# Optimization experiments

Hardware: AMD Instinct MI355X
Metric: run time of the kernel (lower is better)

Reference implementation:

```python
import jax, jax.numpy as jnp
import numpy as np

B, C, T, D = 4, 248, 500, 64


def setup_inputs() -> dict:
    key = jax.random.key(0)
    ks = jax.random.split(key, 7)
    scale = 1.0  # nn.Linear(1, d) default init is U(-1, 1); exact dist irrelevant for correctness baseline
    return {
        "x": jax.random.normal(ks[0], (B, C, T), dtype=jnp.float32),
        "wq": jax.random.uniform(ks[1], (D,), jnp.float32, -scale, scale),
        "bq": jax.random.uniform(ks[2], (D,), jnp.float32, -scale, scale),
        "wk": jax.random.uniform(ks[3], (D,), jnp.float32, -scale, scale),
        "bk": jax.random.uniform(ks[4], (D,), jnp.float32, -scale, scale),
        "wv": jax.random.uniform(ks[5], (D,), jnp.float32, -scale, scale),
        "bv": jax.random.uniform(ks[6], (D,), jnp.float32, -scale, scale),
    }


def reference(x, wq, bq, wk, bk, wv, bv):
    # x: [B, C, T] -> xt: [B, T, C]; each scalar projected to attn_dim D
    xt = jnp.transpose(x, (0, 2, 1))
    Q = xt[..., None] * wq + bq            # [B, T, C, D]
    K = xt[..., None] * wk + bk            # [B, T, C, D]
    V = xt[..., None] * wv + bv            # [B, T, C, D]
    d = Q.shape[-1]
    # channel-wise attention per (B, T) slice
    scores = jnp.einsum("btcd,bted->btce", Q, K) / jnp.sqrt(jnp.float32(d))
    wts = jax.nn.softmax(scores, axis=-1)  # [B, T, C, C] (dropout=0 / eval mode)
    out = jnp.einsum("btce,bted->btcd", wts, V).mean(axis=2)  # [B, T, D]
    return out, wts
```

## Files before the change

### kernel.cpp

```cpp
#include <hip/hip_runtime.h>
#include <math.h>

#define BB 4
#define CC 248
#define TT 500
#define DD 64

__device__ __forceinline__ float waveReduceSum(float v) {
    #pragma unroll
    for (int off = 32; off > 0; off >>= 1) v += __shfl_xor(v, off, 64);
    return v;
}

__global__ __launch_bounds__(256) void csa_kernel(
    const float* __restrict__ x,
    const float* __restrict__ wq, const float* __restrict__ bq,
    const float* __restrict__ wk, const float* __restrict__ bk,
    const float* __restrict__ wv, const float* __restrict__ bv,
    float* __restrict__ out, float* __restrict__ wts)
{
    const int bt = blockIdx.x;
    const int b  = bt / TT;
    const int t  = bt % TT;
    const int tid  = threadIdx.x;
    const int wave = tid >> 6;
    const int lane = tid & 63;

    __shared__ __align__(16) float xs[CC];
    __shared__ float sred[8];
    __shared__ float sA, sB2, sXmax, sXmin, sYbar;

    if (tid < CC) xs[tid] = x[((size_t)b * CC + tid) * TT + t];

    if (wave == 1) {
        float wkv = wk[lane];
        float pa = wq[lane] * wkv;
        float pb = bq[lane] * wkv;
        #pragma unroll
        for (int off = 32; off > 0; off >>= 1) {
            pa += __shfl_xor(pa, off, 64);
            pb += __shfl_xor(pb, off, 64);
        }
        if (lane == 0) { sA = pa * 0.125f; sB2 = pb * 0.125f; }
    }
    __syncthreads();

    float vmax = -INFINITY, vmin = INFINITY;
    if (tid < CC) { vmax = xs[tid]; vmin = xs[tid]; }
    #pragma unroll
    for (int off = 32; off > 0; off >>= 1) {
        vmax = fmaxf(vmax, __shfl_xor(vmax, off, 64));
        vmin = fminf(vmin, __shfl_xor(vmin, off, 64));
    }
    if (lane == 0) { sred[wave] = vmax; sred[4 + wave] = vmin; }
    __syncthreads();
    if (tid == 0) {
        sXmax = fmaxf(fmaxf(sred[0], sred[1]), fmaxf(sred[2], sred[3]));
        sXmin = fminf(fminf(sred[4], sred[5]), fminf(sred[6], sred[7]));
    }
    __syncthreads();

    const float a    = sA;
    const float b2   = sB2;
    const float xmax = sXmax;
    const float xmin = sXmin;
    const float4* xs4 = reinterpret_cast<const float4*>(xs);

    float4 xv = make_float4(0.f, 0.f, 0.f, 0.f);
    const bool active = (lane < CC / 4);
    if (active) xv = xs4[lane];

    float ywave = 0.f;
    const size_t slice = (size_t)bt * CC * CC;

    for (int c = wave; c < CC; c += 4) {
        const float sc = fmaf(a, xs[c], b2);
        const float m  = (sc >= 0.f) ? sc * xmax : sc * xmin;

        float4 p = make_float4(0.f, 0.f, 0.f, 0.f);
        float sum = 0.f, xp = 0.f;
        if (active) {
            p.x = __expf(fmaf(sc, xv.x, -m));
            p.y = __expf(fmaf(sc, xv.y, -m));
            p.z = __expf(fmaf(sc, xv.z, -m));
            p.w = __expf(fmaf(sc, xv.w, -m));
            sum = (p.x + p.y) + (p.z + p.w);
            xp  = (p.x * xv.x + p.y * xv.y) + (p.z * xv.z + p.w * xv.w);
        }
        const float denom = waveReduceSum(sum);
        const float xps   = waveReduceSum(xp);
        const float inv   = 1.0f / denom;

        if (active) {
            float4 o;
            o.x = p.x * inv; o.y = p.y * inv; o.z = p.z * inv; o.w = p.w * inv;
            reinterpret_cast<float4*>(wts + slice + (size_t)c * CC)[lane] = o;
        }
        ywave += xps * inv;
    }

    if (lane == 0) sred[wave] = ywave;
    __syncthreads();
    if (tid == 0)
        sYbar = (sred[0] + sred[1] + sred[2] + sred[3]) * (1.0f / CC);
    __syncthreads();

    if (tid < DD)
        out[(size_t)bt * DD + tid] = fmaf(wv[tid], sYbar, bv[tid]);
}

extern "C" void kernel_launch(void* const* d_in, const int* in_sizes, int n_in,
                              void* d_out, int out_size, void* d_ws, size_t ws_size,
                              hipStream_t stream) {
    const float* x  = (const float*)d_in[0];
    const float* wq = (const float*)d_in[1];
    const float* bq = (const float*)d_in[2];
    const float* wk = (const float*)d_in[3];
    const float* bk = (const float*)d_in[4];
    const float* wv = (const float*)d_in[5];
    const float* bv = (const float*)d_in[6];

    float* out = (float*)d_out;
    float* wts = (float*)d_out + (size_t)BB * TT * DD;

    csa_kernel<<<dim3(BB * TT), dim3(256), 0, stream>>>(x, wq, bq, wk, bk, wv, bv, out, wts);
}
```

Measured before the change: 118.5 us.

## Process two softmax rows per wave with half-wave reductions and exp2

Each wave now splits into two 32-lane halves that each handle one row of the channel-attention softmax, with every lane holding 8 columns instead of 4. This removes the idle lanes from the old 62-of-64 lane mapping and cuts the cross-lane shuffle reductions per row from six steps to five. The score scale is premultiplied by log2(e) so that exp2 can be used directly, and the reciprocal of the sum uses the hardware rcp instead of a full division, which trades a little accuracy for fewer instructions. The loop is unrolled by 2, which may raise register use.

```diff
diff --git a/kernel.cpp b/kernel.cpp
--- a/kernel.cpp
+++ b/kernel.cpp
@@ -6,11 +6,7 @@
 #define TT 500
 #define DD 64
 
-__device__ __forceinline__ float waveReduceSum(float v) {
-    #pragma unroll
-    for (int off = 32; off > 0; off >>= 1) v += __shfl_xor(v, off, 64);
-    return v;
-}
+typedef float f32x4 __attribute__((ext_vector_type(4)));
 
 __global__ __launch_bounds__(256) void csa_kernel(
     const float* __restrict__ x,
@@ -25,6 +21,8 @@
     const int tid  = threadIdx.x;
     const int wave = tid >> 6;
     const int lane = tid & 63;
+    const int q    = lane & 31;
+    const int h    = lane >> 5;
 
     __shared__ __align__(16) float xs[CC];
     __shared__ float sred[8];
@@ -46,7 +44,7 @@
     __syncthreads();
 
     float vmax = -INFINITY, vmin = INFINITY;
-    if (tid < CC) { vmax = xs[tid]; vmin = xs[tid]; }
+    if (tid < CC) { vmax = xs[tid]; vmin = vmax; }
     #pragma unroll
     for (int off = 32; off > 0; off >>= 1) {
         vmax = fmaxf(vmax, __shfl_xor(vmax, off, 64));
@@ -60,49 +58,67 @@
     }
     __syncthreads();
 
-    const float a    = sA;
-    const float b2   = sB2;
+    const float LOG2E = 1.4426950408889634f;
+    const float a2   = sA  * LOG2E;
+    const float b22  = sB2 * LOG2E;
     const float xmax = sXmax;
     const float xmin = sXmin;
-    const float4* xs4 = reinterpret_cast<const float4*>(xs);
 
-    float4 xv = make_float4(0.f, 0.f, 0.f, 0.f);
-    const bool active = (lane < CC / 4);
-    if (active) xv = xs4[lane];
+    const f32x4* xs4 = reinterpret_cast<const f32x4*>(xs);
+    const bool act = (q < 31);
+    f32x4 xlo = {0.f,0.f,0.f,0.f}, xhi = {0.f,0.f,0.f,0.f};
+    if (act) { xlo = xs4[q]; xhi = xs4[31 + q]; }
 
-    float ywave = 0.f;
-    const size_t slice = (size_t)bt * CC * CC;
+    float ysum = 0.f;
+    const size_t slice = (size_t)bt * (CC * CC);
 
-    for (int c = wave; c < CC; c += 4) {
-        const float sc = fmaf(a, xs[c], b2);
-        const float m  = (sc >= 0.f) ? sc * xmax : sc * xmin;
+    #pragma unroll 2
+    for (int i = 0; i < 31; ++i) {
+        const int r = 8 * i + 2 * wave + h;
+        const float scl = fmaf(a2, xs[r], b22);
+        const float ml  = (scl >= 0.f) ? scl * xmax : scl * xmin;
 
-        float4 p = make_float4(0.f, 0.f, 0.f, 0.f);
+        f32x4 plo = {0.f,0.f,0.f,0.f}, phi = {0.f,0.f,0.f,0.f};
         float sum = 0.f, xp = 0.f;
-        if (active) {
-            p.x = __expf(fmaf(sc, xv.x, -m));
-            p.y = __expf(fmaf(sc, xv.y, -m));
-            p.z = __expf(fmaf(sc, xv.z, -m));
-            p.w = __expf(fmaf(sc, xv.w, -m));
-            sum = (p.x + p.y) + (p.z + p.w);
-            xp  = (p.x * xv.x + p.y * xv.y) + (p.z * xv.z + p.w * xv.w);
+        if (act) {
+            plo.x = __builtin_amdgcn_exp2f(fmaf(scl, xlo.x, -ml));
+            plo.y = __builtin_amdgcn_exp2f(fmaf(scl, xlo.y, -ml));
+            plo.z = __builtin_amdgcn_exp2f(fmaf(scl, xlo.z, -ml));
+            plo.w = __builtin_amdgcn_exp2f(fmaf(scl, xlo.w, -ml));
+            phi.x = __builtin_amdgcn_exp2f(fmaf(scl, xhi.x, -ml));
+            phi.y = __builtin_amdgcn_exp2f(fmaf(scl, xhi.y, -ml));
+            phi.z = __builtin_amdgcn_exp2f(fmaf(scl, xhi.z, -ml));
+            phi.w = __builtin_amdgcn_exp2f(fmaf(scl, xhi.w, -ml));
+            sum = ((plo.x + plo.y) + (plo.z + plo.w)) + ((phi.x + phi.y) + (phi.z + phi.w));
+            xp  = ((plo.x * xlo.x + plo.y * xlo.y) + (plo.z * xlo.z + plo.w * xlo.w))
+                + ((phi.x * xhi.x + phi.y * xhi.y) + (phi.z * xhi.z + phi.w * xhi.w));
         }
-        const float denom = waveReduceSum(sum);
-        const float xps   = waveReduceSum(xp);
-        const float inv   = 1.0f / denom;
+        #pragma unroll
+        for (int off = 16; off > 0; off >>= 1) {
+            sum += __shfl_xor(sum, off, 64);
+            xp  += __shfl_xor(xp,  off, 64);
+        }
+        const float inv = __builtin_amdgcn_rcpf(sum);
 
-        if (active) {
-            float4 o;
-            o.x = p.x * inv; o.y = p.y * inv; o.z = p.z * inv; o.w = p.w * inv;
-            reinterpret_cast<float4*>(wts + slice + (size_t)c * CC)[lane] = o;
+        if (act) {
+            f32x4 olo, ohi;
+            olo.x = plo.x * inv; olo.y = plo.y * inv; olo.z = plo.z * inv; olo.w = plo.w * inv;
+            ohi.x = phi.x * inv; ohi.y = phi.y * inv; ohi.z = phi.z * inv; ohi.w = phi.w * inv;
+            f32x4* dst = reinterpret_cast<f32x4*>(wts + slice + (size_t)r * CC);
+            dst[q]      = olo;
+            dst[31 + q] = ohi;
         }
-        ywave += xps * inv;
+        ysum += xp * inv;
     }
 
-    if (lane == 0) sred[wave] = ywave;
+    if (q == 0) sred[wave * 2 + h] = ysum;
     __syncthreads();
-    if (tid == 0)
-        sYbar = (sred[0] + sred[1] + sred[2] + sred[3]) * (1.0f / CC);
+    if (tid == 0) {
+        float s = 0.f;
+        #pragma unroll
+        for (int k = 0; k < 8; ++k) s += sred[k];
+        sYbar = s * (1.0f / CC);
+    }
     __syncthreads();
 
     if (tid < DD)
```

Measured after the change: 104.5 us. 1.13x faster.

## Compute softmax row stats per thread, then write weights in a flat coalesced pass

Applied to the files above, without the earlier changes.

Each thread now owns one softmax row and computes its max-shifted denominator and weighted x sum serially over channels, with no per-row wave reductions. The row parameters go to shared memory, and a second flat pass recomputes the exponentials and writes the weight matrix contiguously using all lanes. It also switches to exp2 with a pre-scaled log2e and a hardware reciprocal. The cost is computing exponentials twice and reading from LDS with divide-by-62 indexing.

```diff
diff --git a/kernel.cpp b/kernel.cpp
--- a/kernel.cpp
+++ b/kernel.cpp
@@ -5,12 +5,9 @@
 #define CC 248
 #define TT 500
 #define DD 64
+#define NQ (CC * CC / 4)
 
-__device__ __forceinline__ float waveReduceSum(float v) {
-    #pragma unroll
-    for (int off = 32; off > 0; off >>= 1) v += __shfl_xor(v, off, 64);
-    return v;
-}
+typedef float f32x4 __attribute__((ext_vector_type(4)));
 
 __global__ __launch_bounds__(256) void csa_kernel(
     const float* __restrict__ x,
@@ -27,6 +24,7 @@
     const int lane = tid & 63;
 
     __shared__ __align__(16) float xs[CC];
+    __shared__ __align__(16) f32x4 sRowV[CC];
     __shared__ float sred[8];
     __shared__ float sA, sB2, sXmax, sXmin, sYbar;
 
@@ -46,7 +44,7 @@
     __syncthreads();
 
     float vmax = -INFINITY, vmin = INFINITY;
-    if (tid < CC) { vmax = xs[tid]; vmin = xs[tid]; }
+    if (tid < CC) { vmax = xs[tid]; vmin = vmax; }
     #pragma unroll
     for (int off = 32; off > 0; off >>= 1) {
         vmax = fmaxf(vmax, __shfl_xor(vmax, off, 64));
@@ -60,50 +58,80 @@
     }
     __syncthreads();
 
-    const float a    = sA;
-    const float b2   = sB2;
+    const float LOG2E = 1.4426950408889634f;
+    const float a2   = sA  * LOG2E;
+    const float b22  = sB2 * LOG2E;
     const float xmax = sXmax;
     const float xmin = sXmin;
-    const float4* xs4 = reinterpret_cast<const float4*>(xs);
+    const f32x4* xs4 = reinterpret_cast<const f32x4*>(xs);
 
-    float4 xv = make_float4(0.f, 0.f, 0.f, 0.f);
-    const bool active = (lane < CC / 4);
-    if (active) xv = xs4[lane];
+    const int  r      = tid;
+    const bool rowact = (r < CC);
+    const float xr = rowact ? xs[r] : 0.f;
+    const float s2 = fmaf(a2, xr, b22);
+    const float m2 = (s2 >= 0.f) ? s2 * xmax : s2 * xmin;
 
-    float ywave = 0.f;
-    const size_t slice = (size_t)bt * CC * CC;
-
-    for (int c = wave; c < CC; c += 4) {
-        const float sc = fmaf(a, xs[c], b2);
-        const float m  = (sc >= 0.f) ? sc * xmax : sc * xmin;
-
-        float4 p = make_float4(0.f, 0.f, 0.f, 0.f);
-        float sum = 0.f, xp = 0.f;
-        if (active) {
-            p.x = __expf(fmaf(sc, xv.x, -m));
-            p.y = __expf(fmaf(sc, xv.y, -m));
-            p.z = __expf(fmaf(sc, xv.z, -m));
-            p.w = __expf(fmaf(sc, xv.w, -m));
-            sum = (p.x + p.y) + (p.z + p.w);
-            xp  = (p.x * xv.x + p.y * xv.y) + (p.z * xv.z + p.w * xv.w);
-        }
-        const float denom = waveReduceSum(sum);
-        const float xps   = waveReduceSum(xp);
-        const float inv   = 1.0f / denom;
-
-        if (active) {
-            float4 o;
-            o.x = p.x * inv; o.y = p.y * inv; o.z = p.z * inv; o.w = p.w * inv;
-            reinterpret_cast<float4*>(wts + slice + (size_t)c * CC)[lane] = o;
-        }
-        ywave += xps * inv;
+    float d0 = 0.f, d1 = 0.f, d2 = 0.f, d3 = 0.f;
+    float p0 = 0.f, p1 = 0.f, p2 = 0.f, p3 = 0.f;
+    #pragma unroll 2
+    for (int j = 0; j < CC / 4; ++j) {
+        const f32x4 xv = xs4[j];
+        const float e0 = __builtin_amdgcn_exp2f(fmaf(s2, xv.x, -m2));
+        const float e1 = __builtin_amdgcn_exp2f(fmaf(s2, xv.y, -m2));
+        const float e2 = __builtin_amdgcn_exp2f(fmaf(s2, xv.z, -m2));
+        const float e3 = __builtin_amdgcn_exp2f(fmaf(s2, xv.w, -m2));
+        d0 += e0; d1 += e1; d2 += e2; d3 += e3;
+        p0 = fmaf(e0, xv.x, p0); p1 = fmaf(e1, xv.y, p1);
+        p2 = fmaf(e2, xv.z, p2); p3 = fmaf(e3, xv.w, p3);
+    }
+    const float denom = (d0 + d1) + (d2 + d3);
+    const float xp    = (p0 + p1) + (p2 + p3);
+    const float inv   = __builtin_amdgcn_rcpf(denom);
+    if (rowact) {
+        f32x4 prm; prm.x = s2; prm.y = -m2; prm.z = inv; prm.w = 0.f;
+        sRowV[r] = prm;
     }
 
-    if (lane == 0) sred[wave] = ywave;
+    float yr = rowact ? xp * inv : 0.f;
+    #pragma unroll
+    for (int off = 32; off > 0; off >>= 1) yr += __shfl_xor(yr, off, 64);
+    if (lane == 0) sred[wave] = yr;
     __syncthreads();
     if (tid == 0)
         sYbar = (sred[0] + sred[1] + sred[2] + sred[3]) * (1.0f / CC);
     __syncthreads();
+
+    f32x4* wq4 = reinterpret_cast<f32x4*>(wts + (size_t)bt * (CC * CC));
+
+    #pragma unroll 2
+    for (int it = 0; it < NQ / 256; ++it) {
+        const int idx = it * 256 + tid;
+        const int row = idx / 62;
+        const int c4  = idx - row * 62;
+        const f32x4 prm = sRowV[row];
+        const f32x4 xv  = xs4[c4];
+        f32x4 o;
+        o.x = __builtin_amdgcn_exp2f(fmaf(prm.x, xv.x, prm.y)) * prm.z;
+        o.y = __builtin_amdgcn_exp2f(fmaf(prm.x, xv.y, prm.y)) * prm.z;
+        o.z = __builtin_amdgcn_exp2f(fmaf(prm.x, xv.z, prm.y)) * prm.z;
+        o.w = __builtin_amdgcn_exp2f(fmaf(prm.x, xv.w, prm.y)) * prm.z;
+        wq4[idx] = o;
+    }
+    {
+        const int idx = (NQ / 256) * 256 + tid;
+        if (tid < NQ - (NQ / 256) * 256) {
+            const int row = idx / 62;
+            const int c4  = idx - row * 62;
+            const f32x4 prm = sRowV[row];
+            const f32x4 xv  = xs4[c4];
+            f32x4 o;
+            o.x = __builtin_amdgcn_exp2f(fmaf(prm.x, xv.x, prm.y)) * prm.z;
+            o.y = __builtin_amdgcn_exp2f(fmaf(prm.x, xv.y, prm.y)) * prm.z;
+            o.z = __builtin_amdgcn_exp2f(fmaf(prm.x, xv.z, prm.y)) * prm.z;
+            o.w = __builtin_amdgcn_exp2f(fmaf(prm.x, xv.w, prm.y)) * prm.z;
+            wq4[idx] = o;
+        }
+    }
 
     if (tid < DD)
         out[(size_t)bt * DD + tid] = fmaf(wv[tid], sYbar, bv[tid]);
```

Result: faster. 105.0 us (-11.4%).
